# Kernel optimization log

Measured on AMD Instinct MI355X. Metric: run time of the kernel, lower is better.

The kernel has to match this reference:

```python
import jax, jax.numpy as jnp
import numpy as np

B, TE, TD, D, U = 8, 256, 256, 256, 256


def setup_inputs() -> dict:
    key = jax.random.key(0)
    k1, k2, k3, k4, k5 = jax.random.split(key, 5)
    glorot = lambda k, shape: jax.random.uniform(
        k, shape, jnp.float32,
        -np.sqrt(6.0 / (shape[0] + shape[1])), np.sqrt(6.0 / (shape[0] + shape[1])))
    return {
        "en_seq": jax.random.normal(k1, (B, TE, D), jnp.float32),
        "de_seq": jax.random.normal(k2, (B, TD, D), jnp.float32),
        "w_en": glorot(k3, (D, U)),
        "w_de": glorot(k4, (D, U)),
        "nu": glorot(k5, (U, 1)),
    }


def reference(en_seq, de_seq, w_en, w_de, nu):
    # Additive co-attention scores.
    ae = jnp.einsum('bte,eu->btu', en_seq, w_en)          # (B, Te, U)
    ad = jnp.einsum('bsd,du->bsu', de_seq, w_de)          # (B, Td, U)
    # co_m[b, td, te, u] = ae[b, te, u] + ad[b, td, u]  (matches K.repeat / repeat_elements layout)
    co = jnp.tanh(ad[:, :, None, :] + ae[:, None, :, :])  # (B, Td, Te, U)
    mu = jnp.einsum('bstu,ul->bst', co, nu)               # (B, Td, Te)
    alphas = jax.nn.softmax(mu, axis=-1)                  # softmax over en time
    max_mu = jnp.max(mu, axis=-1)                         # (B, Td)
    max_alphas = jax.nn.softmax(max_mu, axis=-1)          # softmax over de time
    h_hat = jnp.sum(de_seq * max_alphas[..., None], axis=1)  # (B, Dd)
    sum_en = jnp.einsum('bst,bte->bse', alphas, en_seq)      # (B, Td, De)
    output = jnp.concatenate(
        [de_seq, sum_en, de_seq * sum_en, de_seq * h_hat[:, None, :]], axis=-1)
    return output  # (B, Td, 4*D)
```

## Files before the change

kernel.cpp:

```cpp
#include <hip/hip_runtime.h>

#define B_   8
#define TE_  256
#define TD_  256
#define D_   256
#define U_   256

#define EET_OFF   0
#define ED_OFF    524288
#define MAXMU_OFF 1048576

__device__ __forceinline__ float fexp2(float x) {
#if __has_builtin(__builtin_amdgcn_exp2f)
  return __builtin_amdgcn_exp2f(x);
#else
  return exp2f(x);
#endif
}
__device__ __forceinline__ float frcp(float x) {
#if __has_builtin(__builtin_amdgcn_rcpf)
  return __builtin_amdgcn_rcpf(x);
#else
  return 1.0f / x;
#endif
}

#define LOG2E_F 1.4426950408889634f
#define TWO_LOG2E_F 2.8853900817779268f

__global__ __launch_bounds__(256) void coatt_k1_proj(
    const float* __restrict__ en, const float* __restrict__ de,
    const float* __restrict__ w_en, const float* __restrict__ w_de,
    float* __restrict__ ws) {
  const int which = blockIdx.z;
  const float* __restrict__ A = which ? de : en;
  const float* __restrict__ W = which ? w_de : w_en;
  const int rowBase = blockIdx.y * 64;
  const int colBase = blockIdx.x * 64;
  __shared__ float smem[2][2][32][69];
  const int tid = threadIdx.x;
  const int tx = tid & 15, ty = tid >> 4;
  const int aRow0 = tid >> 3, aC4 = tid & 7;
  const int bK0 = tid >> 4, bC4 = tid & 15;
  float4 aR[2], bR[2];

#pragma unroll
  for (int kk = 0; kk < 2; ++kk) {
    aR[kk] = *(const float4*)&A[(size_t)(rowBase + aRow0 + 32 * kk) * D_ + aC4 * 4];
    bR[kk] = *(const float4*)&W[(size_t)(bK0 + 16 * kk) * U_ + colBase + bC4 * 4];
  }
#pragma unroll
  for (int kk = 0; kk < 2; ++kk) {
    float v[4]; *(float4*)v = aR[kk];
#pragma unroll
    for (int j = 0; j < 4; ++j) smem[0][0][aC4 * 4 + j][aRow0 + 32 * kk] = v[j];
    *(float4*)&smem[1][0][bK0 + 16 * kk][bC4 * 4] = bR[kk];
  }
  __syncthreads();

  float acc[4][4] = {};
#define K1_COMPUTE(BUF)                                              \
  _Pragma("unroll")                                                  \
  for (int k = 0; k < 32; ++k) {                                     \
    float av[4], bv[4];                                              \
    *(float4*)av = *(const float4*)&smem[0][BUF][k][ty * 4];         \
    *(float4*)bv = *(const float4*)&smem[1][BUF][k][tx * 4];         \
    _Pragma("unroll")                                                \
    for (int i = 0; i < 4; ++i)                                      \
      _Pragma("unroll")                                              \
      for (int j = 0; j < 4; ++j)                                    \
        acc[i][j] = fmaf(av[i], bv[j], acc[i][j]);                   \
  }

  for (int kc = 0; kc < 7; ++kc) {
    const int k0 = (kc + 1) * 32;
#pragma unroll
    for (int kk = 0; kk < 2; ++kk) {
      aR[kk] = *(const float4*)&A[(size_t)(rowBase + aRow0 + 32 * kk) * D_ + k0 + aC4 * 4];
      bR[kk] = *(const float4*)&W[(size_t)(k0 + bK0 + 16 * kk) * U_ + colBase + bC4 * 4];
    }
    const int cur = kc & 1, nxt = cur ^ 1;
    K1_COMPUTE(cur)
#pragma unroll
    for (int kk = 0; kk < 2; ++kk) {
      float v[4]; *(float4*)v = aR[kk];
#pragma unroll
      for (int j = 0; j < 4; ++j) smem[0][nxt][aC4 * 4 + j][aRow0 + 32 * kk] = v[j];
      *(float4*)&smem[1][nxt][bK0 + 16 * kk][bC4 * 4] = bR[kk];
    }
    __syncthreads();
  }
  K1_COMPUTE(1)

  if (which) {
    float* __restrict__ outp = ws + ED_OFF;
#pragma unroll
    for (int i = 0; i < 4; ++i) {
      float4 o;
      o.x = fexp2(acc[i][0] * TWO_LOG2E_F);
      o.y = fexp2(acc[i][1] * TWO_LOG2E_F);
      o.z = fexp2(acc[i][2] * TWO_LOG2E_F);
      o.w = fexp2(acc[i][3] * TWO_LOG2E_F);
      *(float4*)&outp[(size_t)(rowBase + ty * 4 + i) * U_ + colBase + tx * 4] = o;
    }
  } else {
    __syncthreads();
    float* Cs = &smem[0][0][0][0];
#pragma unroll
    for (int i = 0; i < 4; ++i)
#pragma unroll
      for (int j = 0; j < 4; ++j)
        Cs[(tx * 4 + j) * 69 + ty * 4 + i] = fexp2(acc[i][j] * TWO_LOG2E_F);
    __syncthreads();
    float* __restrict__ outp = ws + EET_OFF;
    const int b = rowBase >> 8, t0 = rowBase & 255;
    const int u4Base = colBase >> 2;
#pragma unroll
    for (int kk = 0; kk < 4; ++kk) {
      const int q = tid + 256 * kk;
      const int u4l = q >> 6, tl = q & 63;
      float4 v;
      v.x = Cs[(u4l * 4 + 0) * 69 + tl];
      v.y = Cs[(u4l * 4 + 1) * 69 + tl];
      v.z = Cs[(u4l * 4 + 2) * 69 + tl];
      v.w = Cs[(u4l * 4 + 3) * 69 + tl];
      *(float4*)&outp[(size_t)((b * 64 + u4Base + u4l) * 256 + t0 + tl) * 4] = v;
    }
  }
}

__global__ __launch_bounds__(512) void coatt_k24(
    const float* __restrict__ en, const float* __restrict__ de,
    const float* __restrict__ nu, float* __restrict__ ws,
    float* __restrict__ out) {
  const float* __restrict__ EeT = ws + EET_OFF;
  const float* __restrict__ Ed = ws + ED_OFF;
  float* __restrict__ maxmu = ws + MAXMU_OFF;
  const int id = blockIdx.x;
  const int b = id & 7;
  const int sBase = (id >> 3) * 4;
  const int tid = threadIdx.x;
  const int t = tid & 255;
  const int half = tid >> 8;
  const int w = tid >> 6, lane = tid & 63;

  __shared__ float eds[4][256];
  __shared__ float nus[256];
  __shared__ float als[4][256];
  __shared__ float tp[2][4][256];
  __shared__ float part[2][8];

  {
    const float2* src = (const float2*)(Ed + (size_t)(b * TD_ + sBase) * U_);
    ((float2*)&eds[0][0])[tid] = src[tid];
    if (tid < 128) ((float2*)nus)[tid] = ((const float2*)nu)[tid];
  }
  __syncthreads();

  const float* __restrict__ Ee_b = EeT + (size_t)b * (U_ * TE_) + t * 4;
  const int s0 = half * 2;
  float accA0 = 0.f, accB0 = 0.f, accA1 = 0.f, accB1 = 0.f;
#pragma unroll 4
  for (int u4 = 0; u4 < 64; ++u4) {
    const float4 ee4 = *(const float4*)&Ee_b[u4 * 1024];
    const float4 nv = *(const float4*)&nus[u4 * 4];
    const float4 d0 = *(const float4*)&eds[s0][u4 * 4];
    const float4 d1 = *(const float4*)&eds[s0 + 1][u4 * 4];
    const float* eep = (const float*)&ee4;
    const float* nvp = (const float*)&nv;
    const float* p0 = (const float*)&d0;
    const float* p1 = (const float*)&d1;
#pragma unroll
    for (int j = 0; j < 4; ++j) {
      const float r0 = frcp(fmaf(p0[j], eep[j], 1.0f));
      const float r1 = frcp(fmaf(p1[j], eep[j], 1.0f));
      if (j & 1) {
        accB0 = fmaf(nvp[j], r0, accB0);
        accB1 = fmaf(nvp[j], r1, accB1);
      } else {
        accA0 = fmaf(nvp[j], r0, accA0);
        accA1 = fmaf(nvp[j], r1, accA1);
      }
    }
  }
  float v0 = -2.f * (accA0 + accB0);
  float v1 = -2.f * (accA1 + accB1);

  float m0 = v0, m1 = v1;
#pragma unroll
  for (int off = 32; off > 0; off >>= 1) {
    m0 = fmaxf(m0, __shfl_xor(m0, off));
    m1 = fmaxf(m1, __shfl_xor(m1, off));
  }
  if (lane == 0) { part[0][w] = m0; part[1][w] = m1; }
  __syncthreads();
  const int wb = half * 4;
  m0 = fmaxf(fmaxf(part[0][wb], part[0][wb + 1]), fmaxf(part[0][wb + 2], part[0][wb + 3]));
  m1 = fmaxf(fmaxf(part[1][wb], part[1][wb + 1]), fmaxf(part[1][wb + 2], part[1][wb + 3]));
  __syncthreads();
  const float e0 = fexp2((v0 - m0) * LOG2E_F);
  const float e1 = fexp2((v1 - m1) * LOG2E_F);
  float sm0 = e0, sm1 = e1;
#pragma unroll
  for (int off = 32; off > 0; off >>= 1) {
    sm0 += __shfl_xor(sm0, off);
    sm1 += __shfl_xor(sm1, off);
  }
  if (lane == 0) { part[0][w] = sm0; part[1][w] = sm1; }
  __syncthreads();
  const float tot0 = (part[0][wb] + part[0][wb + 1]) + (part[0][wb + 2] + part[0][wb + 3]);
  const float tot1 = (part[1][wb] + part[1][wb + 1]) + (part[1][wb + 2] + part[1][wb + 3]);
  als[s0][t] = e0 * frcp(tot0);
  als[s0 + 1][t] = e1 * frcp(tot1);
  if (t == 0) {
    maxmu[b * TD_ + sBase + s0] = m0;
    maxmu[b * TD_ + sBase + s0 + 1] = m1;
  }
  __syncthreads();

  const int d = t;
  const int tBeg = half * 128;
  const float* __restrict__ en_b = en + (size_t)b * TE_ * D_ + d;
  float sa0 = 0.f, sa1 = 0.f, sa2 = 0.f, sa3 = 0.f;
#pragma unroll 4
  for (int t4 = 0; t4 < 32; ++t4) {
    const int tt = tBeg + t4 * 4;
    const float4 a0 = *(const float4*)&als[0][tt];
    const float4 a1 = *(const float4*)&als[1][tt];
    const float4 a2 = *(const float4*)&als[2][tt];
    const float4 a3 = *(const float4*)&als[3][tt];
    float env[4];
#pragma unroll
    for (int j = 0; j < 4; ++j) env[j] = en_b[(size_t)(tt + j) * D_];
    const float* q0 = (const float*)&a0;
    const float* q1 = (const float*)&a1;
    const float* q2 = (const float*)&a2;
    const float* q3 = (const float*)&a3;
#pragma unroll
    for (int j = 0; j < 4; ++j) {
      sa0 = fmaf(q0[j], env[j], sa0);
      sa1 = fmaf(q1[j], env[j], sa1);
      sa2 = fmaf(q2[j], env[j], sa2);
      sa3 = fmaf(q3[j], env[j], sa3);
    }
  }
  tp[half][0][d] = sa0;
  tp[half][1][d] = sa1;
  tp[half][2][d] = sa2;
  tp[half][3][d] = sa3;
  __syncthreads();
#pragma unroll
  for (int k = 0; k < 2; ++k) {
    const int sl = s0 + k;
    const float se = tp[0][sl][d] + tp[1][sl][d];
    const int s = sBase + sl;
    const float dd = de[(size_t)(b * TD_ + s) * D_ + d];
    float* o = out + (size_t)(b * TD_ + s) * (4 * D_);
    o[d] = dd;
    o[D_ + d] = se;
    o[2 * D_ + d] = dd * se;
  }
}

__global__ __launch_bounds__(256) void coatt_k3_hhat(
    const float* __restrict__ de, const float* __restrict__ ws,
    float* __restrict__ out) {
  const float* __restrict__ maxmu = ws + MAXMU_OFF;
  const int b = blockIdx.y;
  const int dBase = blockIdx.x * 32;
  const int tid = threadIdx.x;
  const int w = tid >> 6, lane = tid & 63;
  __shared__ float red[8];
  __shared__ float malpha[256];
  __shared__ float acc_red[256];
  __shared__ float hh_s[32];
  const float vv = maxmu[b * TD_ + tid];
  float m = vv;
#pragma unroll
  for (int off = 32; off > 0; off >>= 1) m = fmaxf(m, __shfl_xor(m, off));
  if (lane == 0) red[w] = m;
  __syncthreads();
  m = fmaxf(fmaxf(red[0], red[1]), fmaxf(red[2], red[3]));
  const float e = fexp2((vv - m) * LOG2E_F);
  float sm = e;
#pragma unroll
  for (int off = 32; off > 0; off >>= 1) sm += __shfl_xor(sm, off);
  if (lane == 0) red[4 + w] = sm;
  __syncthreads();
  sm = (red[4] + red[5]) + (red[6] + red[7]);
  malpha[tid] = e * frcp(sm);
  __syncthreads();
  const int dl = tid & 31, sg = tid >> 5;
  float acc = 0.f;
  for (int s = sg * 32; s < sg * 32 + 32; ++s)
    acc = fmaf(de[(size_t)(b * TD_ + s) * D_ + dBase + dl], malpha[s], acc);
  acc_red[tid] = acc;
  __syncthreads();
  if (tid < 32) {
    float tsum = acc_red[tid];
#pragma unroll
    for (int g = 1; g < 8; ++g) tsum += acc_red[g * 32 + tid];
    hh_s[tid] = tsum;
  }
  __syncthreads();
  const float hh = hh_s[dl];
#pragma unroll 4
  for (int s = sg; s < TD_; s += 8) {
    const float dd = de[(size_t)(b * TD_ + s) * D_ + dBase + dl];
    out[(size_t)(b * TD_ + s) * (4 * D_) + 3 * D_ + dBase + dl] = dd * hh;
  }
}

extern "C" void kernel_launch(void* const* d_in, const int* in_sizes, int n_in,
                              void* d_out, int out_size, void* d_ws, size_t ws_size,
                              hipStream_t stream) {
  (void)in_sizes; (void)n_in; (void)out_size; (void)ws_size;
  const float* en   = (const float*)d_in[0];
  const float* de   = (const float*)d_in[1];
  const float* w_en = (const float*)d_in[2];
  const float* w_de = (const float*)d_in[3];
  const float* nu   = (const float*)d_in[4];
  float* out = (float*)d_out;
  float* ws  = (float*)d_ws;

  coatt_k1_proj<<<dim3(4, 32, 2), 256, 0, stream>>>(en, de, w_en, w_de, ws);
  coatt_k24<<<dim3(512), 512, 0, stream>>>(en, de, nu, ws, out);
  coatt_k3_hhat<<<dim3(8, 8), 256, 0, stream>>>(de, ws, out);
}
```

Measured before the change: 112.7 us.

## Fuse three kernels into one persistent kernel with software grid barriers

Merges the projection GEMM, the score/softmax/context stage and the h_hat stage into a single 512-block kernel, separated by atomic-counter grid barriers. This removes two kernel launches and their gaps. In exchange, the projection stage now runs on 256 blocks with only half of each block's threads computing. The h_hat softmax and reduction are also recomputed redundantly in every block. The barrier relies on all 512 blocks being co-resident, which deadlocks if occupancy is lower than expected.

```diff
diff --git a/kernel.cpp b/kernel.cpp
--- a/kernel.cpp
+++ b/kernel.cpp
@@ -28,144 +28,168 @@
 #define LOG2E_F 1.4426950408889634f
 #define TWO_LOG2E_F 2.8853900817779268f
 
-__global__ __launch_bounds__(256) void coatt_k1_proj(
+#define NBLOCKS 512
+
+__device__ int g_cnt;
+__device__ int g_gen;
+
+__device__ __forceinline__ void gridbar() {
+  __syncthreads();
+  if (threadIdx.x == 0) {
+    __threadfence();
+    const int gen = __hip_atomic_load(&g_gen, __ATOMIC_RELAXED, __HIP_MEMORY_SCOPE_AGENT);
+    const int old = __hip_atomic_fetch_add(&g_cnt, 1, __ATOMIC_ACQ_REL, __HIP_MEMORY_SCOPE_AGENT);
+    if (old == NBLOCKS - 1) {
+      __hip_atomic_store(&g_cnt, 0, __ATOMIC_RELAXED, __HIP_MEMORY_SCOPE_AGENT);
+      __hip_atomic_fetch_add(&g_gen, 1, __ATOMIC_RELEASE, __HIP_MEMORY_SCOPE_AGENT);
+    } else {
+      while (__hip_atomic_load(&g_gen, __ATOMIC_ACQUIRE, __HIP_MEMORY_SCOPE_AGENT) == gen)
+        __builtin_amdgcn_s_sleep(2);
+    }
+    __threadfence();
+  }
+  __syncthreads();
+}
+
+__global__ __launch_bounds__(512, 4) void coatt_fused(
     const float* __restrict__ en, const float* __restrict__ de,
     const float* __restrict__ w_en, const float* __restrict__ w_de,
-    float* __restrict__ ws) {
-  const int which = blockIdx.z;
-  const float* __restrict__ A = which ? de : en;
-  const float* __restrict__ W = which ? w_de : w_en;
-  const int rowBase = blockIdx.y * 64;
-  const int colBase = blockIdx.x * 64;
-  __shared__ float smem[2][2][32][69];
-  const int tid = threadIdx.x;
-  const int tx = tid & 15, ty = tid >> 4;
-  const int aRow0 = tid >> 3, aC4 = tid & 7;
-  const int bK0 = tid >> 4, bC4 = tid & 15;
-  float4 aR[2], bR[2];
-
-#pragma unroll
-  for (int kk = 0; kk < 2; ++kk) {
-    aR[kk] = *(const float4*)&A[(size_t)(rowBase + aRow0 + 32 * kk) * D_ + aC4 * 4];
-    bR[kk] = *(const float4*)&W[(size_t)(bK0 + 16 * kk) * U_ + colBase + bC4 * 4];
-  }
-#pragma unroll
-  for (int kk = 0; kk < 2; ++kk) {
-    float v[4]; *(float4*)v = aR[kk];
-#pragma unroll
-    for (int j = 0; j < 4; ++j) smem[0][0][aC4 * 4 + j][aRow0 + 32 * kk] = v[j];
-    *(float4*)&smem[1][0][bK0 + 16 * kk][bC4 * 4] = bR[kk];
-  }
-  __syncthreads();
-
-  float acc[4][4] = {};
-#define K1_COMPUTE(BUF)                                              \
-  _Pragma("unroll")                                                  \
-  for (int k = 0; k < 32; ++k) {                                     \
-    float av[4], bv[4];                                              \
-    *(float4*)av = *(const float4*)&smem[0][BUF][k][ty * 4];         \
-    *(float4*)bv = *(const float4*)&smem[1][BUF][k][tx * 4];         \
-    _Pragma("unroll")                                                \
-    for (int i = 0; i < 4; ++i)                                      \
-      _Pragma("unroll")                                              \
-      for (int j = 0; j < 4; ++j)                                    \
-        acc[i][j] = fmaf(av[i], bv[j], acc[i][j]);                   \
-  }
-
-  for (int kc = 0; kc < 7; ++kc) {
-    const int k0 = (kc + 1) * 32;
-#pragma unroll
-    for (int kk = 0; kk < 2; ++kk) {
-      aR[kk] = *(const float4*)&A[(size_t)(rowBase + aRow0 + 32 * kk) * D_ + k0 + aC4 * 4];
-      bR[kk] = *(const float4*)&W[(size_t)(k0 + bK0 + 16 * kk) * U_ + colBase + bC4 * 4];
-    }
-    const int cur = kc & 1, nxt = cur ^ 1;
-    K1_COMPUTE(cur)
-#pragma unroll
-    for (int kk = 0; kk < 2; ++kk) {
-      float v[4]; *(float4*)v = aR[kk];
-#pragma unroll
-      for (int j = 0; j < 4; ++j) smem[0][nxt][aC4 * 4 + j][aRow0 + 32 * kk] = v[j];
-      *(float4*)&smem[1][nxt][bK0 + 16 * kk][bC4 * 4] = bR[kk];
-    }
-    __syncthreads();
-  }
-  K1_COMPUTE(1)
-
-  if (which) {
-    float* __restrict__ outp = ws + ED_OFF;
-#pragma unroll
-    for (int i = 0; i < 4; ++i) {
-      float4 o;
-      o.x = fexp2(acc[i][0] * TWO_LOG2E_F);
-      o.y = fexp2(acc[i][1] * TWO_LOG2E_F);
-      o.z = fexp2(acc[i][2] * TWO_LOG2E_F);
-      o.w = fexp2(acc[i][3] * TWO_LOG2E_F);
-      *(float4*)&outp[(size_t)(rowBase + ty * 4 + i) * U_ + colBase + tx * 4] = o;
-    }
-  } else {
-    __syncthreads();
-    float* Cs = &smem[0][0][0][0];
-#pragma unroll
-    for (int i = 0; i < 4; ++i)
-#pragma unroll
-      for (int j = 0; j < 4; ++j)
-        Cs[(tx * 4 + j) * 69 + ty * 4 + i] = fexp2(acc[i][j] * TWO_LOG2E_F);
-    __syncthreads();
-    float* __restrict__ outp = ws + EET_OFF;
-    const int b = rowBase >> 8, t0 = rowBase & 255;
-    const int u4Base = colBase >> 2;
-#pragma unroll
-    for (int kk = 0; kk < 4; ++kk) {
-      const int q = tid + 256 * kk;
-      const int u4l = q >> 6, tl = q & 63;
-      float4 v;
-      v.x = Cs[(u4l * 4 + 0) * 69 + tl];
-      v.y = Cs[(u4l * 4 + 1) * 69 + tl];
-      v.z = Cs[(u4l * 4 + 2) * 69 + tl];
-      v.w = Cs[(u4l * 4 + 3) * 69 + tl];
-      *(float4*)&outp[(size_t)((b * 64 + u4Base + u4l) * 256 + t0 + tl) * 4] = v;
-    }
-  }
-}
-
-__global__ __launch_bounds__(512) void coatt_k24(
-    const float* __restrict__ en, const float* __restrict__ de,
     const float* __restrict__ nu, float* __restrict__ ws,
     float* __restrict__ out) {
-  const float* __restrict__ EeT = ws + EET_OFF;
-  const float* __restrict__ Ed = ws + ED_OFF;
+  __shared__ union {
+    struct { float s[2][2][32][69]; } k1;
+    struct {
+      float eds[4][256];
+      float nus[256];
+      float als[4][256];
+      float tp[2][4][256];
+      float part[2][8];
+      float red[16];
+    } k24;
+  } sm;
+
+  const int id = blockIdx.x;
+  const int tid = threadIdx.x;
+  float* __restrict__ eet = ws + EET_OFF;
+  float* __restrict__ edp = ws + ED_OFF;
   float* __restrict__ maxmu = ws + MAXMU_OFF;
-  const int id = blockIdx.x;
+
+  if (id < 256) {
+    const int which = id >> 7;
+    const int rem = id & 127;
+    const int colBase = (rem & 3) * 64;
+    const int rowBase = (rem >> 2) * 64;
+    const float* __restrict__ A = which ? de : en;
+    const float* __restrict__ W = which ? w_de : w_en;
+    const int aRow = tid >> 3, aC4 = tid & 7;
+    const int bK = tid >> 4, bC4 = tid & 15;
+    const int tx = tid & 15, ty = (tid >> 4) & 15;
+    const bool comp = tid < 256;
+
+    float4 aR = *(const float4*)&A[(size_t)(rowBase + aRow) * D_ + aC4 * 4];
+    float4 bR = *(const float4*)&W[(size_t)bK * U_ + colBase + bC4 * 4];
+    {
+      float v[4]; *(float4*)v = aR;
+#pragma unroll
+      for (int j = 0; j < 4; ++j) sm.k1.s[0][0][aC4 * 4 + j][aRow] = v[j];
+      *(float4*)&sm.k1.s[1][0][bK][bC4 * 4] = bR;
+    }
+    __syncthreads();
+
+    float acc[4][4] = {};
+#define K1_COMPUTE(BUF)                                                  \
+    if (comp) {                                                          \
+      _Pragma("unroll")                                                  \
+      for (int k = 0; k < 32; ++k) {                                     \
+        float av[4], bv[4];                                              \
+        *(float4*)av = *(const float4*)&sm.k1.s[0][BUF][k][ty * 4];      \
+        *(float4*)bv = *(const float4*)&sm.k1.s[1][BUF][k][tx * 4];      \
+        _Pragma("unroll")                                                \
+        for (int i = 0; i < 4; ++i)                                      \
+          _Pragma("unroll")                                              \
+          for (int j = 0; j < 4; ++j)                                    \
+            acc[i][j] = fmaf(av[i], bv[j], acc[i][j]);                   \
+      }                                                                  \
+    }
+
+    for (int kc = 0; kc < 7; ++kc) {
+      const int k0 = (kc + 1) * 32;
+      aR = *(const float4*)&A[(size_t)(rowBase + aRow) * D_ + k0 + aC4 * 4];
+      bR = *(const float4*)&W[(size_t)(k0 + bK) * U_ + colBase + bC4 * 4];
+      const int cur = kc & 1, nxt = cur ^ 1;
+      K1_COMPUTE(cur)
+      {
+        float v[4]; *(float4*)v = aR;
+#pragma unroll
+        for (int j = 0; j < 4; ++j) sm.k1.s[0][nxt][aC4 * 4 + j][aRow] = v[j];
+        *(float4*)&sm.k1.s[1][nxt][bK][bC4 * 4] = bR;
+      }
+      __syncthreads();
+    }
+    K1_COMPUTE(1)
+
+    if (which) {
+      if (comp) {
+#pragma unroll
+        for (int i = 0; i < 4; ++i) {
+          float4 o;
+          o.x = fexp2(acc[i][0] * TWO_LOG2E_F);
+          o.y = fexp2(acc[i][1] * TWO_LOG2E_F);
+          o.z = fexp2(acc[i][2] * TWO_LOG2E_F);
+          o.w = fexp2(acc[i][3] * TWO_LOG2E_F);
+          *(float4*)&edp[(size_t)(rowBase + ty * 4 + i) * U_ + colBase + tx * 4] = o;
+        }
+      }
+    } else {
+      __syncthreads();
+      float* Cs = &sm.k1.s[0][0][0][0];
+      if (comp) {
+#pragma unroll
+        for (int i = 0; i < 4; ++i)
+#pragma unroll
+          for (int j = 0; j < 4; ++j)
+            Cs[(tx * 4 + j) * 69 + ty * 4 + i] = fexp2(acc[i][j] * TWO_LOG2E_F);
+      }
+      __syncthreads();
+      const int b = rowBase >> 8, t0 = rowBase & 255;
+      const int u4Base = colBase >> 2;
+#pragma unroll
+      for (int kk = 0; kk < 2; ++kk) {
+        const int q = tid + 512 * kk;
+        const int u4l = q >> 6, tl = q & 63;
+        float4 v;
+        v.x = Cs[(u4l * 4 + 0) * 69 + tl];
+        v.y = Cs[(u4l * 4 + 1) * 69 + tl];
+        v.z = Cs[(u4l * 4 + 2) * 69 + tl];
+        v.w = Cs[(u4l * 4 + 3) * 69 + tl];
+        *(float4*)&eet[(size_t)((b * 64 + u4Base + u4l) * 256 + t0 + tl) * 4] = v;
+      }
+    }
+  }
+
+  gridbar();
+
   const int b = id & 7;
   const int sBase = (id >> 3) * 4;
-  const int tid = threadIdx.x;
   const int t = tid & 255;
   const int half = tid >> 8;
   const int w = tid >> 6, lane = tid & 63;
-
-  __shared__ float eds[4][256];
-  __shared__ float nus[256];
-  __shared__ float als[4][256];
-  __shared__ float tp[2][4][256];
-  __shared__ float part[2][8];
-
   {
-    const float2* src = (const float2*)(Ed + (size_t)(b * TD_ + sBase) * U_);
-    ((float2*)&eds[0][0])[tid] = src[tid];
-    if (tid < 128) ((float2*)nus)[tid] = ((const float2*)nu)[tid];
-  }
-  __syncthreads();
-
-  const float* __restrict__ Ee_b = EeT + (size_t)b * (U_ * TE_) + t * 4;
+    const float2* src = (const float2*)(edp + (size_t)(b * TD_ + sBase) * U_);
+    ((float2*)&sm.k24.eds[0][0])[tid] = src[tid];
+    if (tid < 128) ((float2*)sm.k24.nus)[tid] = ((const float2*)nu)[tid];
+  }
+  __syncthreads();
+
+  const float* __restrict__ Ee_b = eet + (size_t)b * (U_ * TE_) + t * 4;
   const int s0 = half * 2;
   float accA0 = 0.f, accB0 = 0.f, accA1 = 0.f, accB1 = 0.f;
 #pragma unroll 4
   for (int u4 = 0; u4 < 64; ++u4) {
     const float4 ee4 = *(const float4*)&Ee_b[u4 * 1024];
-    const float4 nv = *(const float4*)&nus[u4 * 4];
-    const float4 d0 = *(const float4*)&eds[s0][u4 * 4];
-    const float4 d1 = *(const float4*)&eds[s0 + 1][u4 * 4];
+    const float4 nv = *(const float4*)&sm.k24.nus[u4 * 4];
+    const float4 d0 = *(const float4*)&sm.k24.eds[s0][u4 * 4];
+    const float4 d1 = *(const float4*)&sm.k24.eds[s0 + 1][u4 * 4];
     const float* eep = (const float*)&ee4;
     const float* nvp = (const float*)&nv;
     const float* p0 = (const float*)&d0;
@@ -192,11 +216,13 @@
     m0 = fmaxf(m0, __shfl_xor(m0, off));
     m1 = fmaxf(m1, __shfl_xor(m1, off));
   }
-  if (lane == 0) { part[0][w] = m0; part[1][w] = m1; }
+  if (lane == 0) { sm.k24.part[0][w] = m0; sm.k24.part[1][w] = m1; }
   __syncthreads();
   const int wb = half * 4;
-  m0 = fmaxf(fmaxf(part[0][wb], part[0][wb + 1]), fmaxf(part[0][wb + 2], part[0][wb + 3]));
-  m1 = fmaxf(fmaxf(part[1][wb], part[1][wb + 1]), fmaxf(part[1][wb + 2], part[1][wb + 3]));
+  m0 = fmaxf(fmaxf(sm.k24.part[0][wb], sm.k24.part[0][wb + 1]),
+             fmaxf(sm.k24.part[0][wb + 2], sm.k24.part[0][wb + 3]));
+  m1 = fmaxf(fmaxf(sm.k24.part[1][wb], sm.k24.part[1][wb + 1]),
+             fmaxf(sm.k24.part[1][wb + 2], sm.k24.part[1][wb + 3]));
   __syncthreads();
   const float e0 = fexp2((v0 - m0) * LOG2E_F);
   const float e1 = fexp2((v1 - m1) * LOG2E_F);
@@ -206,108 +232,106 @@
     sm0 += __shfl_xor(sm0, off);
     sm1 += __shfl_xor(sm1, off);
   }
-  if (lane == 0) { part[0][w] = sm0; part[1][w] = sm1; }
-  __syncthreads();
-  const float tot0 = (part[0][wb] + part[0][wb + 1]) + (part[0][wb + 2] + part[0][wb + 3]);
-  const float tot1 = (part[1][wb] + part[1][wb + 1]) + (part[1][wb + 2] + part[1][wb + 3]);
-  als[s0][t] = e0 * frcp(tot0);
-  als[s0 + 1][t] = e1 * frcp(tot1);
+  if (lane == 0) { sm.k24.part[0][w] = sm0; sm.k24.part[1][w] = sm1; }
+  __syncthreads();
+  const float tot0 = (sm.k24.part[0][wb] + sm.k24.part[0][wb + 1]) +
+                     (sm.k24.part[0][wb + 2] + sm.k24.part[0][wb + 3]);
+  const float tot1 = (sm.k24.part[1][wb] + sm.k24.part[1][wb + 1]) +
+                     (sm.k24.part[1][wb + 2] + sm.k24.part[1][wb + 3]);
+  sm.k24.als[s0][t] = e0 * frcp(tot0);
+  sm.k24.als[s0 + 1][t] = e1 * frcp(tot1);
   if (t == 0) {
     maxmu[b * TD_ + sBase + s0] = m0;
     maxmu[b * TD_ + sBase + s0 + 1] = m1;
   }
   __syncthreads();
 
-  const int d = t;
-  const int tBeg = half * 128;
-  const float* __restrict__ en_b = en + (size_t)b * TE_ * D_ + d;
-  float sa0 = 0.f, sa1 = 0.f, sa2 = 0.f, sa3 = 0.f;
+  {
+    const int d = t;
+    const int tBeg = half * 128;
+    const float* __restrict__ en_b = en + (size_t)b * TE_ * D_ + d;
+    float sa0 = 0.f, sa1 = 0.f, sa2 = 0.f, sa3 = 0.f;
 #pragma unroll 4
-  for (int t4 = 0; t4 < 32; ++t4) {
-    const int tt = tBeg + t4 * 4;
-    const float4 a0 = *(const float4*)&als[0][tt];
-    const float4 a1 = *(const float4*)&als[1][tt];
-    const float4 a2 = *(const float4*)&als[2][tt];
-    const float4 a3 = *(const float4*)&als[3][tt];
-    float env[4];
-#pragma unroll
-    for (int j = 0; j < 4; ++j) env[j] = en_b[(size_t)(tt + j) * D_];
-    const float* q0 = (const float*)&a0;
-    const float* q1 = (const float*)&a1;
-    const float* q2 = (const float*)&a2;
-    const float* q3 = (const float*)&a3;
-#pragma unroll
-    for (int j = 0; j < 4; ++j) {
-      sa0 = fmaf(q0[j], env[j], sa0);
-      sa1 = fmaf(q1[j], env[j], sa1);
-      sa2 = fmaf(q2[j], env[j], sa2);
-      sa3 = fmaf(q3[j], env[j], sa3);
-    }
-  }
-  tp[half][0][d] = sa0;
-  tp[half][1][d] = sa1;
-  tp[half][2][d] = sa2;
-  tp[half][3][d] = sa3;
-  __syncthreads();
-#pragma unroll
-  for (int k = 0; k < 2; ++k) {
-    const int sl = s0 + k;
-    const float se = tp[0][sl][d] + tp[1][sl][d];
-    const int s = sBase + sl;
-    const float dd = de[(size_t)(b * TD_ + s) * D_ + d];
-    float* o = out + (size_t)(b * TD_ + s) * (4 * D_);
-    o[d] = dd;
-    o[D_ + d] = se;
-    o[2 * D_ + d] = dd * se;
-  }
-}
-
-__global__ __launch_bounds__(256) void coatt_k3_hhat(
-    const float* __restrict__ de, const float* __restrict__ ws,
-    float* __restrict__ out) {
-  const float* __restrict__ maxmu = ws + MAXMU_OFF;
-  const int b = blockIdx.y;
-  const int dBase = blockIdx.x * 32;
-  const int tid = threadIdx.x;
-  const int w = tid >> 6, lane = tid & 63;
-  __shared__ float red[8];
-  __shared__ float malpha[256];
-  __shared__ float acc_red[256];
-  __shared__ float hh_s[32];
-  const float vv = maxmu[b * TD_ + tid];
-  float m = vv;
-#pragma unroll
-  for (int off = 32; off > 0; off >>= 1) m = fmaxf(m, __shfl_xor(m, off));
-  if (lane == 0) red[w] = m;
-  __syncthreads();
-  m = fmaxf(fmaxf(red[0], red[1]), fmaxf(red[2], red[3]));
-  const float e = fexp2((vv - m) * LOG2E_F);
-  float sm = e;
-#pragma unroll
-  for (int off = 32; off > 0; off >>= 1) sm += __shfl_xor(sm, off);
-  if (lane == 0) red[4 + w] = sm;
-  __syncthreads();
-  sm = (red[4] + red[5]) + (red[6] + red[7]);
-  malpha[tid] = e * frcp(sm);
-  __syncthreads();
-  const int dl = tid & 31, sg = tid >> 5;
-  float acc = 0.f;
-  for (int s = sg * 32; s < sg * 32 + 32; ++s)
-    acc = fmaf(de[(size_t)(b * TD_ + s) * D_ + dBase + dl], malpha[s], acc);
-  acc_red[tid] = acc;
-  __syncthreads();
-  if (tid < 32) {
-    float tsum = acc_red[tid];
-#pragma unroll
-    for (int g = 1; g < 8; ++g) tsum += acc_red[g * 32 + tid];
-    hh_s[tid] = tsum;
-  }
-  __syncthreads();
-  const float hh = hh_s[dl];
+    for (int t4 = 0; t4 < 32; ++t4) {
+      const int tt = tBeg + t4 * 4;
+      const float4 a0 = *(const float4*)&sm.k24.als[0][tt];
+      const float4 a1 = *(const float4*)&sm.k24.als[1][tt];
+      const float4 a2 = *(const float4*)&sm.k24.als[2][tt];
+      const float4 a3 = *(const float4*)&sm.k24.als[3][tt];
+      float env[4];
+#pragma unroll
+      for (int j = 0; j < 4; ++j) env[j] = en_b[(size_t)(tt + j) * D_];
+      const float* q0 = (const float*)&a0;
+      const float* q1 = (const float*)&a1;
+      const float* q2 = (const float*)&a2;
+      const float* q3 = (const float*)&a3;
+#pragma unroll
+      for (int j = 0; j < 4; ++j) {
+        sa0 = fmaf(q0[j], env[j], sa0);
+        sa1 = fmaf(q1[j], env[j], sa1);
+        sa2 = fmaf(q2[j], env[j], sa2);
+        sa3 = fmaf(q3[j], env[j], sa3);
+      }
+    }
+    sm.k24.tp[half][0][d] = sa0;
+    sm.k24.tp[half][1][d] = sa1;
+    sm.k24.tp[half][2][d] = sa2;
+    sm.k24.tp[half][3][d] = sa3;
+    __syncthreads();
+#pragma unroll
+    for (int k = 0; k < 2; ++k) {
+      const int sl = s0 + k;
+      const float se = sm.k24.tp[0][sl][d] + sm.k24.tp[1][sl][d];
+      const int s = sBase + sl;
+      const float dd = de[(size_t)(b * TD_ + s) * D_ + d];
+      float* o = out + (size_t)(b * TD_ + s) * (4 * D_);
+      o[d] = dd;
+      o[D_ + d] = se;
+      o[2 * D_ + d] = dd * se;
+    }
+  }
+
+  gridbar();
+
+  {
+    float* ma = sm.k24.als[0];
+    float* red = sm.k24.red;
+    if (tid < 256) {
+      const float vv = maxmu[b * TD_ + tid];
+      float m = vv;
+#pragma unroll
+      for (int off = 32; off > 0; off >>= 1) m = fmaxf(m, __shfl_xor(m, off));
+      if (lane == 0) red[w] = m;
+      __syncthreads();
+      m = fmaxf(fmaxf(red[0], red[1]), fmaxf(red[2], red[3]));
+      const float e = fexp2((vv - m) * LOG2E_F);
+      float s = e;
+#pragma unroll
+      for (int off = 32; off > 0; off >>= 1) s += __shfl_xor(s, off);
+      if (lane == 0) red[8 + w] = s;
+      __syncthreads();
+      s = (red[8] + red[9]) + (red[10] + red[11]);
+      ma[tid] = e * frcp(s);
+    } else {
+      __syncthreads();
+      __syncthreads();
+    }
+    __syncthreads();
+    const int d = t;
+    float acc = 0.f;
+    const float* __restrict__ de_b = de + (size_t)b * TD_ * D_ + d;
 #pragma unroll 4
-  for (int s = sg; s < TD_; s += 8) {
-    const float dd = de[(size_t)(b * TD_ + s) * D_ + dBase + dl];
-    out[(size_t)(b * TD_ + s) * (4 * D_) + 3 * D_ + dBase + dl] = dd * hh;
+    for (int s = half * 128; s < half * 128 + 128; ++s)
+      acc = fmaf(de_b[(size_t)s * D_], ma[s], acc);
+    sm.k24.tp[half][0][d] = acc;
+    __syncthreads();
+    const float hh = sm.k24.tp[0][0][d] + sm.k24.tp[1][0][d];
+#pragma unroll
+    for (int k = 0; k < 2; ++k) {
+      const int s = sBase + half * 2 + k;
+      const float dd = de[(size_t)(b * TD_ + s) * D_ + d];
+      out[(size_t)(b * TD_ + s) * (4 * D_) + 3 * D_ + d] = dd * hh;
+    }
   }
 }
 
@@ -323,7 +347,5 @@
   float* out = (float*)d_out;
   float* ws  = (float*)d_ws;
 
-  coatt_k1_proj<<<dim3(4, 32, 2), 256, 0, stream>>>(en, de, w_en, w_de, ws);
-  coatt_k24<<<dim3(512), 512, 0, stream>>>(en, de, nu, ws, out);
-  coatt_k3_hhat<<<dim3(8, 8), 256, 0, stream>>>(de, ws, out);
-}
+  coatt_fused<<<dim3(NBLOCKS), 512, 0, stream>>>(en, de, w_en, w_de, nu, ws, out);
+}
```

Measured after the change: 319.4 us. 184% more time.

## Drop LDS staging in projection GEMM and read Ed/nu directly from global

Applied to the files above, without the earlier changes.

The projection kernel no longer double-buffers A and W tiles through shared memory. Each thread now loads its operands straight from global memory and relies on the caches, which removes the LDS stores and block barriers from the K loop. In the scoring kernel, Ed rows and nu are read directly from global with a wave-uniform base (readfirstlane), so they can use scalar or broadcast loads instead of an LDS prologue and barrier. The cost is more global and cache traffic in the GEMM, with uncoalesced per-row A loads.

```diff
diff --git a/kernel.cpp b/kernel.cpp
--- a/kernel.cpp
+++ b/kernel.cpp
@@ -31,69 +31,38 @@
 __global__ __launch_bounds__(256) void coatt_k1_proj(
     const float* __restrict__ en, const float* __restrict__ de,
     const float* __restrict__ w_en, const float* __restrict__ w_de,
-    float* __restrict__ ws) {
+    float* __restrict__ eet, float* __restrict__ edp) {
   const int which = blockIdx.z;
   const float* __restrict__ A = which ? de : en;
   const float* __restrict__ W = which ? w_de : w_en;
   const int rowBase = blockIdx.y * 64;
   const int colBase = blockIdx.x * 64;
-  __shared__ float smem[2][2][32][69];
+  __shared__ float Cs[64][69];
   const int tid = threadIdx.x;
   const int tx = tid & 15, ty = tid >> 4;
-  const int aRow0 = tid >> 3, aC4 = tid & 7;
-  const int bK0 = tid >> 4, bC4 = tid & 15;
-  float4 aR[2], bR[2];
-
-#pragma unroll
-  for (int kk = 0; kk < 2; ++kk) {
-    aR[kk] = *(const float4*)&A[(size_t)(rowBase + aRow0 + 32 * kk) * D_ + aC4 * 4];
-    bR[kk] = *(const float4*)&W[(size_t)(bK0 + 16 * kk) * U_ + colBase + bC4 * 4];
-  }
-#pragma unroll
-  for (int kk = 0; kk < 2; ++kk) {
-    float v[4]; *(float4*)v = aR[kk];
-#pragma unroll
-    for (int j = 0; j < 4; ++j) smem[0][0][aC4 * 4 + j][aRow0 + 32 * kk] = v[j];
-    *(float4*)&smem[1][0][bK0 + 16 * kk][bC4 * 4] = bR[kk];
-  }
-  __syncthreads();
 
   float acc[4][4] = {};
-#define K1_COMPUTE(BUF)                                              \
-  _Pragma("unroll")                                                  \
-  for (int k = 0; k < 32; ++k) {                                     \
-    float av[4], bv[4];                                              \
-    *(float4*)av = *(const float4*)&smem[0][BUF][k][ty * 4];         \
-    *(float4*)bv = *(const float4*)&smem[1][BUF][k][tx * 4];         \
-    _Pragma("unroll")                                                \
-    for (int i = 0; i < 4; ++i)                                      \
-      _Pragma("unroll")                                              \
-      for (int j = 0; j < 4; ++j)                                    \
-        acc[i][j] = fmaf(av[i], bv[j], acc[i][j]);                   \
-  }
-
-  for (int kc = 0; kc < 7; ++kc) {
-    const int k0 = (kc + 1) * 32;
-#pragma unroll
-    for (int kk = 0; kk < 2; ++kk) {
-      aR[kk] = *(const float4*)&A[(size_t)(rowBase + aRow0 + 32 * kk) * D_ + k0 + aC4 * 4];
-      bR[kk] = *(const float4*)&W[(size_t)(k0 + bK0 + 16 * kk) * U_ + colBase + bC4 * 4];
-    }
-    const int cur = kc & 1, nxt = cur ^ 1;
-    K1_COMPUTE(cur)
-#pragma unroll
-    for (int kk = 0; kk < 2; ++kk) {
-      float v[4]; *(float4*)v = aR[kk];
-#pragma unroll
-      for (int j = 0; j < 4; ++j) smem[0][nxt][aC4 * 4 + j][aRow0 + 32 * kk] = v[j];
-      *(float4*)&smem[1][nxt][bK0 + 16 * kk][bC4 * 4] = bR[kk];
-    }
-    __syncthreads();
-  }
-  K1_COMPUTE(1)
+#pragma unroll 4
+  for (int k4 = 0; k4 < 64; ++k4) {
+    float a[4][4];
+#pragma unroll
+    for (int i = 0; i < 4; ++i)
+      *(float4*)a[i] =
+          *(const float4*)&A[(size_t)(rowBase + ty * 4 + i) * D_ + k4 * 4];
+#pragma unroll
+    for (int kk = 0; kk < 4; ++kk) {
+      float bv[4];
+      *(float4*)bv =
+          *(const float4*)&W[(size_t)(k4 * 4 + kk) * U_ + colBase + tx * 4];
+#pragma unroll
+      for (int i = 0; i < 4; ++i)
+#pragma unroll
+        for (int j = 0; j < 4; ++j)
+          acc[i][j] = fmaf(a[i][kk], bv[j], acc[i][j]);
+    }
+  }
 
   if (which) {
-    float* __restrict__ outp = ws + ED_OFF;
 #pragma unroll
     for (int i = 0; i < 4; ++i) {
       float4 o;
@@ -101,18 +70,15 @@
       o.y = fexp2(acc[i][1] * TWO_LOG2E_F);
       o.z = fexp2(acc[i][2] * TWO_LOG2E_F);
       o.w = fexp2(acc[i][3] * TWO_LOG2E_F);
-      *(float4*)&outp[(size_t)(rowBase + ty * 4 + i) * U_ + colBase + tx * 4] = o;
+      *(float4*)&edp[(size_t)(rowBase + ty * 4 + i) * U_ + colBase + tx * 4] = o;
     }
   } else {
+#pragma unroll
+    for (int i = 0; i < 4; ++i)
+#pragma unroll
+      for (int j = 0; j < 4; ++j)
+        Cs[tx * 4 + j][ty * 4 + i] = fexp2(acc[i][j] * TWO_LOG2E_F);
     __syncthreads();
-    float* Cs = &smem[0][0][0][0];
-#pragma unroll
-    for (int i = 0; i < 4; ++i)
-#pragma unroll
-      for (int j = 0; j < 4; ++j)
-        Cs[(tx * 4 + j) * 69 + ty * 4 + i] = fexp2(acc[i][j] * TWO_LOG2E_F);
-    __syncthreads();
-    float* __restrict__ outp = ws + EET_OFF;
     const int b = rowBase >> 8, t0 = rowBase & 255;
     const int u4Base = colBase >> 2;
 #pragma unroll
@@ -120,22 +86,20 @@
       const int q = tid + 256 * kk;
       const int u4l = q >> 6, tl = q & 63;
       float4 v;
-      v.x = Cs[(u4l * 4 + 0) * 69 + tl];
-      v.y = Cs[(u4l * 4 + 1) * 69 + tl];
-      v.z = Cs[(u4l * 4 + 2) * 69 + tl];
-      v.w = Cs[(u4l * 4 + 3) * 69 + tl];
-      *(float4*)&outp[(size_t)((b * 64 + u4Base + u4l) * 256 + t0 + tl) * 4] = v;
+      v.x = Cs[u4l * 4 + 0][tl];
+      v.y = Cs[u4l * 4 + 1][tl];
+      v.z = Cs[u4l * 4 + 2][tl];
+      v.w = Cs[u4l * 4 + 3][tl];
+      *(float4*)&eet[(size_t)((b * 64 + u4Base + u4l) * 256 + t0 + tl) * 4] = v;
     }
   }
 }
 
 __global__ __launch_bounds__(512) void coatt_k24(
     const float* __restrict__ en, const float* __restrict__ de,
-    const float* __restrict__ nu, float* __restrict__ ws,
+    const float* __restrict__ nu, const float* __restrict__ eet,
+    const float* __restrict__ edp, float* __restrict__ maxmu,
     float* __restrict__ out) {
-  const float* __restrict__ EeT = ws + EET_OFF;
-  const float* __restrict__ Ed = ws + ED_OFF;
-  float* __restrict__ maxmu = ws + MAXMU_OFF;
   const int id = blockIdx.x;
   const int b = id & 7;
   const int sBase = (id >> 3) * 4;
@@ -144,28 +108,23 @@
   const int half = tid >> 8;
   const int w = tid >> 6, lane = tid & 63;
 
-  __shared__ float eds[4][256];
-  __shared__ float nus[256];
   __shared__ float als[4][256];
   __shared__ float tp[2][4][256];
   __shared__ float part[2][8];
 
-  {
-    const float2* src = (const float2*)(Ed + (size_t)(b * TD_ + sBase) * U_);
-    ((float2*)&eds[0][0])[tid] = src[tid];
-    if (tid < 128) ((float2*)nus)[tid] = ((const float2*)nu)[tid];
-  }
-  __syncthreads();
-
-  const float* __restrict__ Ee_b = EeT + (size_t)b * (U_ * TE_) + t * 4;
-  const int s0 = half * 2;
+  const int edBase =
+      __builtin_amdgcn_readfirstlane((b * TD_ + sBase + half * 2) * U_);
+  const float* __restrict__ Ed0 = edp + edBase;
+  const float* __restrict__ Ed1 = Ed0 + U_;
+  const float* __restrict__ Ee_b = eet + (size_t)b * (U_ * TE_) + t * 4;
+
   float accA0 = 0.f, accB0 = 0.f, accA1 = 0.f, accB1 = 0.f;
 #pragma unroll 4
   for (int u4 = 0; u4 < 64; ++u4) {
     const float4 ee4 = *(const float4*)&Ee_b[u4 * 1024];
-    const float4 nv = *(const float4*)&nus[u4 * 4];
-    const float4 d0 = *(const float4*)&eds[s0][u4 * 4];
-    const float4 d1 = *(const float4*)&eds[s0 + 1][u4 * 4];
+    const float4 nv = *(const float4*)&nu[u4 * 4];
+    const float4 d0 = *(const float4*)&Ed0[u4 * 4];
+    const float4 d1 = *(const float4*)&Ed1[u4 * 4];
     const float* eep = (const float*)&ee4;
     const float* nvp = (const float*)&nv;
     const float* p0 = (const float*)&d0;
@@ -195,8 +154,10 @@
   if (lane == 0) { part[0][w] = m0; part[1][w] = m1; }
   __syncthreads();
   const int wb = half * 4;
-  m0 = fmaxf(fmaxf(part[0][wb], part[0][wb + 1]), fmaxf(part[0][wb + 2], part[0][wb + 3]));
-  m1 = fmaxf(fmaxf(part[1][wb], part[1][wb + 1]), fmaxf(part[1][wb + 2], part[1][wb + 3]));
+  m0 = fmaxf(fmaxf(part[0][wb], part[0][wb + 1]),
+             fmaxf(part[0][wb + 2], part[0][wb + 3]));
+  m1 = fmaxf(fmaxf(part[1][wb], part[1][wb + 1]),
+             fmaxf(part[1][wb + 2], part[1][wb + 3]));
   __syncthreads();
   const float e0 = fexp2((v0 - m0) * LOG2E_F);
   const float e1 = fexp2((v1 - m1) * LOG2E_F);
@@ -208,8 +169,11 @@
   }
   if (lane == 0) { part[0][w] = sm0; part[1][w] = sm1; }
   __syncthreads();
-  const float tot0 = (part[0][wb] + part[0][wb + 1]) + (part[0][wb + 2] + part[0][wb + 3]);
-  const float tot1 = (part[1][wb] + part[1][wb + 1]) + (part[1][wb + 2] + part[1][wb + 3]);
+  const float tot0 = (part[0][wb] + part[0][wb + 1]) +
+                     (part[0][wb + 2] + part[0][wb + 3]);
+  const float tot1 = (part[1][wb] + part[1][wb + 1]) +
+                     (part[1][wb + 2] + part[1][wb + 3]);
+  const int s0 = half * 2;
   als[s0][t] = e0 * frcp(tot0);
   als[s0 + 1][t] = e1 * frcp(tot1);
   if (t == 0) {
@@ -263,9 +227,8 @@
 }
 
 __global__ __launch_bounds__(256) void coatt_k3_hhat(
-    const float* __restrict__ de, const float* __restrict__ ws,
+    const float* __restrict__ de, const float* __restrict__ maxmu,
     float* __restrict__ out) {
-  const float* __restrict__ maxmu = ws + MAXMU_OFF;
   const int b = blockIdx.y;
   const int dBase = blockIdx.x * 32;
   const int tid = threadIdx.x;
@@ -323,7 +286,9 @@
   float* out = (float*)d_out;
   float* ws  = (float*)d_ws;
 
-  coatt_k1_proj<<<dim3(4, 32, 2), 256, 0, stream>>>(en, de, w_en, w_de, ws);
-  coatt_k24<<<dim3(512), 512, 0, stream>>>(en, de, nu, ws, out);
-  coatt_k3_hhat<<<dim3(8, 8), 256, 0, stream>>>(de, ws, out);
-}
+  coatt_k1_proj<<<dim3(4, 32, 2), 256, 0, stream>>>(
+      en, de, w_en, w_de, ws + EET_OFF, ws + ED_OFF);
+  coatt_k24<<<dim3(512), 512, 0, stream>>>(
+      en, de, nu, ws + EET_OFF, ws + ED_OFF, ws + MAXMU_OFF, out);
+  coatt_k3_hhat<<<dim3(8, 8), 256, 0, stream>>>(de, ws + MAXMU_OFF, out);
+}
```

Result: slower. 150.6 us (+33.7%).
